# Optimization experiments

Hardware: AMD Instinct MI355X
Metric: run time of the kernel (lower is better)

Reference implementation:

```python
import jax, jax.numpy as jnp
import numpy as np
import math

H, D = 8, 16
O = H * D  # out_channels = 128
N_TYPES = 2
EDGE_META = [(0, 1), (1, 0)]  # (src_type, dst_type) per edge type: user->item, item->user

def _segment_softmax(alpha, dst, n):
    # PyG softmax over incoming edges grouped by destination node
    amax = jax.ops.segment_max(alpha, dst, num_segments=n)
    amax = jnp.where(jnp.isfinite(amax), amax, 0.0)
    ex = jnp.exp(alpha - amax[dst])
    den = jax.ops.segment_sum(ex, dst, num_segments=n)
    return ex / (den[dst] + 1e-16)

def setup_inputs():
    key = jax.random.key(0)
    ks = jax.random.split(key, 8)
    N, E, I = 50000, 500000, 128
    s = 1.0 / math.sqrt(I)
    sd = 1.0 / math.sqrt(D)
    return {
        "x": jax.random.normal(ks[0], (N_TYPES, N, I), jnp.float32),
        "k_w": jax.random.normal(ks[1], (N_TYPES, O, I), jnp.float32) * s,
        "k_b": jnp.zeros((N_TYPES, O), jnp.float32),
        "q_w": jax.random.normal(ks[2], (N_TYPES, O, I), jnp.float32) * s,
        "q_b": jnp.zeros((N_TYPES, O), jnp.float32),
        "v_w": jax.random.normal(ks[3], (N_TYPES, O, I), jnp.float32) * s,
        "v_b": jnp.zeros((N_TYPES, O), jnp.float32),
        "a_w": jax.random.normal(ks[4], (N_TYPES, O, O), jnp.float32) * s,
        "a_b": jnp.zeros((N_TYPES, O), jnp.float32),
        "skip": jnp.ones((N_TYPES,), jnp.float32),
        "a_rel": jax.random.normal(ks[5], (2, H, D, D), jnp.float32) * sd,
        "m_rel": jax.random.normal(ks[6], (2, H, D, D), jnp.float32) * sd,
        "p_rel": jnp.ones((2, H), jnp.float32),
        "ln_g": jnp.ones((O,), jnp.float32),
        "ln_b": jnp.zeros((O,), jnp.float32),
        "edge_index": jax.random.randint(ks[7], (2, 2, E), 0, N, jnp.int32),
    }

def reference(x, k_w, k_b, q_w, q_b, v_w, v_b, a_w, a_b, skip, a_rel, m_rel, p_rel, ln_g, ln_b, edge_index):
    N = x.shape[1]
    lin = lambda xi, w, b: xi @ w.T + b
    # per-node-type K/Q/V projections -> [T, N, H, D]
    k = jnp.stack([lin(x[t], k_w[t], k_b[t]) for t in range(N_TYPES)]).reshape(N_TYPES, N, H, D)
    q = jnp.stack([lin(x[t], q_w[t], q_b[t]) for t in range(N_TYPES)]).reshape(N_TYPES, N, H, D)
    v = jnp.stack([lin(x[t], v_w[t], v_b[t]) for t in range(N_TYPES)]).reshape(N_TYPES, N, H, D)
    agg = jnp.zeros((N_TYPES, N, O), x.dtype)
    for e, (st, dt) in enumerate(EDGE_META):
        src, dst = edge_index[e, 0], edge_index[e, 1]
        ke = jnp.einsum('nhd,hde->nhe', k[st], a_rel[e])  # relation-transformed keys
        ve = jnp.einsum('nhd,hde->nhe', v[st], m_rel[e])  # relation-transformed values
        alpha = jnp.einsum('ehd,ehd->eh', q[dt][dst], ke[src]) * p_rel[e] / math.sqrt(D)
        alpha = _segment_softmax(alpha, dst, N)  # [E, H]
        msg = (ve[src] * alpha[..., None]).reshape(-1, O)
        agg = agg.at[dt].add(jax.ops.segment_sum(msg, dst, num_segments=N))
    outs = []
    for t in range(N_TYPES):
        o = lin(jax.nn.gelu(agg[t], approximate=False), a_w[t], a_b[t])
        beta = jax.nn.sigmoid(skip[t])
        o = beta * o + (1.0 - beta) * x[t]  # HGT skip (out_channels == in_channels)
        o = jax.nn.relu(o)
        mu = jnp.mean(o, axis=-1, keepdims=True)
        var = jnp.mean((o - mu) ** 2, axis=-1, keepdims=True)
        o = (o - mu) / jnp.sqrt(var + 1e-5) * ln_g + ln_b  # LayerNorm; dropout = identity (eval)
        outs.append(o)
    return jnp.stack(outs)  # [2, N, 128]
```

## Files before the change

kernel.cpp:

```cpp
#include <hip/hip_runtime.h>
#include <math.h>


#define EB_STRIDE 40

typedef __attribute__((ext_vector_type(8))) short short8;
typedef __attribute__((ext_vector_type(4))) float floatx4;

__device__ __forceinline__ float bf2f(unsigned int bits16) {
  union { unsigned int i; float f; } u; u.i = bits16 << 16; return u.f;
}
__device__ __forceinline__ float bf2f_hi(unsigned int u) {
  union { unsigned int i; float f; } v; v.i = u & 0xffff0000u; return v.f;
}
__device__ __forceinline__ unsigned short f2bf(float f) {
  union { float ff; unsigned int i; } u; u.ff = f;
  unsigned int x = u.i;
  x += 0x7fffu + ((x >> 16) & 1u);
  return (unsigned short)(x >> 16);
}

__global__ void fuse_weights(
    const float* __restrict__ k_w, const float* __restrict__ k_b,
    const float* __restrict__ q_w, const float* __restrict__ q_b,
    const float* __restrict__ v_w, const float* __restrict__ v_b,
    const float* __restrict__ a_w, const float* __restrict__ a_b,
    const float* __restrict__ a_rel, const float* __restrict__ m_rel,
    const float* __restrict__ p_rel,
    unsigned short* __restrict__ Wfb, float* __restrict__ Bf)
{
  int tid = blockIdx.x * 256 + threadIdx.x;
  if (tid >= 2 * 4 * 128 * 128) return;
  int t   = tid >> 16;
  int rem = tid & 65535;
  int m   = rem >> 14;
  int o   = (rem >> 7) & 127;
  int i   = rem & 127;
  float w, bias;
  if (m == 0) {
    w    = q_w[t * 16384 + o * 128 + i];
    bias = q_b[t * 128 + o];
  } else if (m == 3) {
    w    = a_w[t * 16384 + o * 128 + i];
    bias = a_b[t * 128 + o];
  } else {
    const float* bw  = (m == 1) ? k_w : v_w;
    const float* bb  = (m == 1) ? k_b : v_b;
    const float* rel = (m == 1) ? a_rel : m_rel;
    int h = o >> 4, eo = o & 15;
    float s = 0.f, sb = 0.f;
    #pragma unroll
    for (int d = 0; d < 16; ++d) {
      float r = rel[t * 2048 + h * 256 + d * 16 + eo];
      s  += bw[t * 16384 + (h * 16 + d) * 128 + i] * r;
      sb += bb[t * 128 + h * 16 + d] * r;
    }
    if (m == 1) {
      float sc = p_rel[t * 8 + h] * 0.25f;
      s *= sc; sb *= sc;
    }
    w = s; bias = sb;
  }
  Wfb[tid] = f2bf(w);
  if (i == 0) Bf[t * 512 + m * 128 + o] = bias;
}

__global__ void init_cnt(int* __restrict__ cnt, int nC)
{
  int tid = blockIdx.x * 256 + threadIdx.x;
  if (tid < nC) cnt[tid] = 0;
}

__global__ void fill_edges(const int* __restrict__ ei, int* __restrict__ cnt,
                           int* __restrict__ ebuf, int N, int E)
{
  int e = blockIdx.y;
  int i = blockIdx.x * 256 + threadIdx.x;
  if (i >= E) return;
  int src = ei[(size_t)e * 2 * E + i];
  int dst = ei[(size_t)e * 2 * E + E + i];
  int b = (1 - e) * N + dst;
  int pos = atomicAdd(&cnt[b], 1);
  if (pos < EB_STRIDE) ebuf[(size_t)b * EB_STRIDE + pos] = src;
}

__global__ __launch_bounds__(256) void gemm_qkv(
    const float* __restrict__ x, const unsigned short* __restrict__ Wfb,
    const float* __restrict__ Bf, unsigned short* __restrict__ qbuf,
    unsigned short* __restrict__ kvbuf, int Nn)
{
  __shared__ alignas(16) unsigned short Als[128][136];
  __shared__ alignas(16) unsigned short Bls[128][136];
  const int tid = threadIdx.x;
  const int t = blockIdx.y;
  const int m0 = blockIdx.x * 128;
  const int lane = tid & 63, w = tid >> 6;
  const int col = lane & 15, quad = lane >> 4;
  const int morder[3] = {1, 2, 0};

  {
    int r = tid & 127, h = tid >> 7;
    int gn = m0 + r;
    if (gn < Nn) {
      const float* ap = x + (size_t)t * Nn * 128 + (size_t)gn * 128 + h * 64;
      #pragma unroll
      for (int j = 0; j < 16; ++j) {
        float4 f = ((const float4*)ap)[j];
        ushort4 s;
        s.x = f2bf(f.x); s.y = f2bf(f.y); s.z = f2bf(f.z); s.w = f2bf(f.w);
        *(ushort4*)&Als[r][h * 64 + j * 4] = s;
      }
    } else {
      ushort4 z = make_ushort4(0, 0, 0, 0);
      #pragma unroll
      for (int j = 0; j < 16; ++j) *(ushort4*)&Als[r][h * 64 + j * 4] = z;
    }
  }

  float acc_k[2][8][4];
  float bias_n[8];

  for (int mi_ = 0; mi_ < 3; ++mi_) {
    int m = morder[mi_];
    __syncthreads();
    {
      int r = tid & 127, h = tid >> 7;
      const unsigned short* wp = Wfb + (((size_t)(t * 4 + m)) << 14) + r * 128 + h * 64;
      #pragma unroll
      for (int j = 0; j < 8; ++j)
        *(uint4*)&Bls[r][h * 64 + j * 8] = ((const uint4*)wp)[j];
    }
    __syncthreads();

    floatx4 acc[2][8];
    #pragma unroll
    for (int mi = 0; mi < 2; ++mi)
      #pragma unroll
      for (int ni = 0; ni < 8; ++ni) acc[mi][ni] = (floatx4)(0.f);

    #pragma unroll
    for (int k0 = 0; k0 < 128; k0 += 32) {
      int kk = k0 + quad * 8;
      short8 a0 = *(const short8*)&Als[w * 32 + col][kk];
      short8 a1 = *(const short8*)&Als[w * 32 + 16 + col][kk];
      #pragma unroll
      for (int ni = 0; ni < 8; ++ni) {
        short8 b = *(const short8*)&Bls[ni * 16 + col][kk];
        acc[0][ni] = __builtin_amdgcn_mfma_f32_16x16x32_bf16(a0, b, acc[0][ni], 0, 0, 0);
        acc[1][ni] = __builtin_amdgcn_mfma_f32_16x16x32_bf16(a1, b, acc[1][ni], 0, 0, 0);
      }
    }

    const float* Bv = Bf + t * 512 + m * 128;
    #pragma unroll
    for (int ni = 0; ni < 8; ++ni) bias_n[ni] = Bv[ni * 16 + col];

    if (m == 1) {
      #pragma unroll
      for (int mi = 0; mi < 2; ++mi)
        #pragma unroll
        for (int ni = 0; ni < 8; ++ni)
          #pragma unroll
          for (int reg = 0; reg < 4; ++reg)
            acc_k[mi][ni][reg] = acc[mi][ni][reg] + bias_n[ni];
    } else if (m == 2) {
      unsigned int* kvp = (unsigned int*)kvbuf + ((size_t)t * Nn) * 128;
      #pragma unroll
      for (int mi = 0; mi < 2; ++mi)
        #pragma unroll
        for (int reg = 0; reg < 4; ++reg) {
          int row = m0 + w * 32 + mi * 16 + quad * 4 + reg;
          if (row >= Nn) continue;
          unsigned int* cp = kvp + (size_t)row * 128 + col;
          #pragma unroll
          for (int ni = 0; ni < 8; ++ni) {
            unsigned int kbits = f2bf(acc_k[mi][ni][reg]);
            unsigned int vbits = f2bf(acc[mi][ni][reg] + bias_n[ni]);
            cp[ni * 16] = (vbits << 16) | kbits;
          }
        }
    } else {
      #pragma unroll
      for (int mi = 0; mi < 2; ++mi)
        #pragma unroll
        for (int reg = 0; reg < 4; ++reg) {
          int row = m0 + w * 32 + mi * 16 + quad * 4 + reg;
          if (row >= Nn) continue;
          unsigned short* cp = qbuf + ((size_t)t * Nn + row) * 128 + col;
          #pragma unroll
          for (int ni = 0; ni < 8; ++ni)
            cp[ni * 16] = f2bf(acc[mi][ni][reg] + bias_n[ni]);
        }
    }
  }
}

__global__ __launch_bounds__(256) void gather_fused(
    const unsigned short* __restrict__ qbuf, const unsigned short* __restrict__ kvbuf,
    const int* __restrict__ cnt, const int* __restrict__ ebuf,
    unsigned short* __restrict__ gbuf, int N)
{
  int wid = (blockIdx.x * 256 + threadIdx.x) >> 6;
  int l = threadIdx.x & 63;
  if (wid >= 2 * N) return;
  int dt = (wid >= N) ? 1 : 0;
  int e  = 1 - dt;
  int deg = cnt[wid]; if (deg > EB_STRIDE) deg = EB_STRIDE;
  int g = l >> 4, gl = l & 15;

  uint4 qr = *(const uint4*)(qbuf + (size_t)wid * 128 + 8 * gl);
  float qv[8];
  qv[0] = bf2f(qr.x & 0xffffu); qv[1] = bf2f(qr.x >> 16);
  qv[2] = bf2f(qr.y & 0xffffu); qv[3] = bf2f(qr.y >> 16);
  qv[4] = bf2f(qr.z & 0xffffu); qv[5] = bf2f(qr.z >> 16);
  qv[6] = bf2f(qr.w & 0xffffu); qv[7] = bf2f(qr.w >> 16);

  const unsigned short* kvbase = kvbuf + ((size_t)e * N) * 256;
  const int* eb = ebuf + (size_t)wid * EB_STRIDE;
  int mysrc = (l < deg) ? eb[l] : 0;

  float acc[8];
  #pragma unroll
  for (int c = 0; c < 8; ++c) acc[c] = 0.f;
  float den = 0.f;

  for (int j0 = 0; j0 < deg; j0 += 4) {
    int j = j0 + g;
    bool valid = j < deg;
    int src = __shfl(mysrc, valid ? j : 0, 64);
    const unsigned short* kv = kvbase + (size_t)src * 256 + 16 * gl;
    uint4 a = *(const uint4*)kv;
    uint4 b = *(const uint4*)(kv + 8);
    float p;
    p = qv[0] * bf2f(a.x & 0xffffu);
    p = fmaf(qv[1], bf2f(a.y & 0xffffu), p);
    p = fmaf(qv[2], bf2f(a.z & 0xffffu), p);
    p = fmaf(qv[3], bf2f(a.w & 0xffffu), p);
    p = fmaf(qv[4], bf2f(b.x & 0xffffu), p);
    p = fmaf(qv[5], bf2f(b.y & 0xffffu), p);
    p = fmaf(qv[6], bf2f(b.z & 0xffffu), p);
    p = fmaf(qv[7], bf2f(b.w & 0xffffu), p);
    float pt = p + __shfl_xor(p, 1, 64);
    float ex = valid ? __expf(pt) : 0.f;
    den += ex;
    acc[0] = fmaf(ex, bf2f_hi(a.x), acc[0]);
    acc[1] = fmaf(ex, bf2f_hi(a.y), acc[1]);
    acc[2] = fmaf(ex, bf2f_hi(a.z), acc[2]);
    acc[3] = fmaf(ex, bf2f_hi(a.w), acc[3]);
    acc[4] = fmaf(ex, bf2f_hi(b.x), acc[4]);
    acc[5] = fmaf(ex, bf2f_hi(b.y), acc[5]);
    acc[6] = fmaf(ex, bf2f_hi(b.z), acc[6]);
    acc[7] = fmaf(ex, bf2f_hi(b.w), acc[7]);
  }

  #pragma unroll
  for (int off = 16; off < 64; off <<= 1) {
    #pragma unroll
    for (int c = 0; c < 8; ++c) acc[c] += __shfl_xor(acc[c], off, 64);
    den += __shfl_xor(den, off, 64);
  }

  if (g == 0) {
    float rden = 1.f / (den + 1e-16f);
    unsigned short r[8];
    #pragma unroll
    for (int c = 0; c < 8; ++c) {
      float gg = acc[c] * rden;
      r[c] = f2bf(0.5f * gg * (1.f + erff(gg * 0.70710678118654752f)));
    }
    unsigned short* op = gbuf + (size_t)wid * 128 + 8 * gl;
    *(ushort4*)op       = make_ushort4(r[0], r[1], r[2], r[3]);
    *(ushort4*)(op + 4) = make_ushort4(r[4], r[5], r[6], r[7]);
  }
}

__global__ __launch_bounds__(256) void gemm_ln(
    const unsigned short* __restrict__ gbuf, const unsigned short* __restrict__ Wfb,
    const float* __restrict__ Bf, const float* __restrict__ x,
    const float* __restrict__ skip, const float* __restrict__ ln_g,
    const float* __restrict__ ln_b, float* __restrict__ outp, int Nn)
{
  __shared__ alignas(16) unsigned short Als[128][136];
  __shared__ alignas(16) unsigned short Bls[128][136];
  const int tid = threadIdx.x;
  const int t = blockIdx.y;
  const int m0 = blockIdx.x * 128;
  const int lane = tid & 63, w = tid >> 6;
  const int col = lane & 15, quad = lane >> 4;

  {
    int r = tid & 127, h = tid >> 7;
    int gn = m0 + r;
    if (gn < Nn) {
      const unsigned short* ap = gbuf + (size_t)t * Nn * 128 + (size_t)gn * 128 + h * 64;
      #pragma unroll
      for (int j = 0; j < 8; ++j)
        *(uint4*)&Als[r][h * 64 + j * 8] = ((const uint4*)ap)[j];
    } else {
      uint4 z = make_uint4(0, 0, 0, 0);
      #pragma unroll
      for (int j = 0; j < 8; ++j) *(uint4*)&Als[r][h * 64 + j * 8] = z;
    }
  }
  {
    int r = tid & 127, h = tid >> 7;
    const unsigned short* wp = Wfb + (((size_t)(t * 4 + 3)) << 14) + r * 128 + h * 64;
    #pragma unroll
    for (int j = 0; j < 8; ++j)
      *(uint4*)&Bls[r][h * 64 + j * 8] = ((const uint4*)wp)[j];
  }
  __syncthreads();

  floatx4 acc[2][8];
  #pragma unroll
  for (int mi = 0; mi < 2; ++mi)
    #pragma unroll
    for (int ni = 0; ni < 8; ++ni) acc[mi][ni] = (floatx4)(0.f);

  #pragma unroll
  for (int k0 = 0; k0 < 128; k0 += 32) {
    int kk = k0 + quad * 8;
    short8 a0 = *(const short8*)&Als[w * 32 + col][kk];
    short8 a1 = *(const short8*)&Als[w * 32 + 16 + col][kk];
    #pragma unroll
    for (int ni = 0; ni < 8; ++ni) {
      short8 b = *(const short8*)&Bls[ni * 16 + col][kk];
      acc[0][ni] = __builtin_amdgcn_mfma_f32_16x16x32_bf16(a0, b, acc[0][ni], 0, 0, 0);
      acc[1][ni] = __builtin_amdgcn_mfma_f32_16x16x32_bf16(a1, b, acc[1][ni], 0, 0, 0);
    }
  }

  const float* Bv = Bf + t * 512 + 3 * 128;
  float bias_n[8], g_n[8], b_n[8];
  #pragma unroll
  for (int ni = 0; ni < 8; ++ni) {
    bias_n[ni] = Bv[ni * 16 + col];
    g_n[ni]    = ln_g[ni * 16 + col];
    b_n[ni]    = ln_b[ni * 16 + col];
  }
  float sv = skip[t];
  float beta = 1.f / (1.f + __expf(-sv));
  const float* xt = x + (size_t)t * Nn * 128;
  float* op = outp + (size_t)t * Nn * 128;

  #pragma unroll
  for (int mi = 0; mi < 2; ++mi)
    #pragma unroll
    for (int reg = 0; reg < 4; ++reg) {
      int row = m0 + w * 32 + mi * 16 + quad * 4 + reg;
      if (row >= Nn) continue;
      const float* xr = xt + (size_t)row * 128;
      float vals[8], s = 0.f;
      #pragma unroll
      for (int ni = 0; ni < 8; ++ni) {
        float o = acc[mi][ni][reg] + bias_n[ni];
        float v = fmaxf(beta * o + (1.f - beta) * xr[ni * 16 + col], 0.f);
        vals[ni] = v; s += v;
      }
      #pragma unroll
      for (int off = 1; off < 16; off <<= 1) s += __shfl_xor(s, off, 64);
      float mu = s * 0.0078125f;
      float sq = 0.f;
      #pragma unroll
      for (int ni = 0; ni < 8; ++ni) { float d = vals[ni] - mu; sq += d * d; }
      #pragma unroll
      for (int off = 1; off < 16; off <<= 1) sq += __shfl_xor(sq, off, 64);
      float rstd = rsqrtf(sq * 0.0078125f + 1e-5f);
      float* orow = op + (size_t)row * 128 + col;
      #pragma unroll
      for (int ni = 0; ni < 8; ++ni)
        orow[ni * 16] = (vals[ni] - mu) * rstd * g_n[ni] + b_n[ni];
    }
}

extern "C" void kernel_launch(void* const* d_in, const int* in_sizes, int n_in,
                              void* d_out, int out_size, void* d_ws, size_t ws_size,
                              hipStream_t stream) {
  const float* x     = (const float*)d_in[0];
  const float* k_w   = (const float*)d_in[1];
  const float* k_b   = (const float*)d_in[2];
  const float* q_w   = (const float*)d_in[3];
  const float* q_b   = (const float*)d_in[4];
  const float* v_w   = (const float*)d_in[5];
  const float* v_b   = (const float*)d_in[6];
  const float* a_w   = (const float*)d_in[7];
  const float* a_b   = (const float*)d_in[8];
  const float* skip  = (const float*)d_in[9];
  const float* a_rel = (const float*)d_in[10];
  const float* m_rel = (const float*)d_in[11];
  const float* p_rel = (const float*)d_in[12];
  const float* ln_g  = (const float*)d_in[13];
  const float* ln_b  = (const float*)d_in[14];
  const int* ei      = (const int*)d_in[15];
  float* out         = (float*)d_out;

  const int N = in_sizes[0] / 256;
  const int E = in_sizes[15] / 4;

  unsigned short* Wfb = (unsigned short*)d_ws;
  float* Bf = (float*)(Wfb + 2 * 4 * 128 * 128);
  unsigned short* qbuf = (unsigned short*)(Bf + 2 * 4 * 128);
  unsigned short* kvbuf = qbuf + (size_t)2 * N * 128;
  int* cnt  = (int*)(kvbuf + (size_t)2 * N * 256);
  int* ebuf = cnt + (size_t)2 * N;
  unsigned short* gbuf = (unsigned short*)(ebuf + (size_t)2 * N * EB_STRIDE);

  fuse_weights<<<(2 * 4 * 128 * 128 + 255) / 256, 256, 0, stream>>>(
      k_w, k_b, q_w, q_b, v_w, v_b, a_w, a_b, a_rel, m_rel, p_rel, Wfb, Bf);

  init_cnt<<<(2 * N + 255) / 256, 256, 0, stream>>>(cnt, 2 * N);

  fill_edges<<<dim3((E + 255) / 256, 2), 256, 0, stream>>>(ei, cnt, ebuf, N, E);

  int Mb = (N + 127) / 128;
  gemm_qkv<<<dim3(Mb, 2), 256, 0, stream>>>(x, Wfb, Bf, qbuf, kvbuf, N);

  gather_fused<<<(2 * N * 64 + 255) / 256, 256, 0, stream>>>(
      qbuf, kvbuf, cnt, ebuf, gbuf, N);

  gemm_ln<<<dim3(Mb, 2), 256, 0, stream>>>(
      gbuf, Wfb, Bf, x, skip, ln_g, ln_b, out, N);
}
```

Measured before the change: 324.9 us.

## Fuse edge bucketing into QKV GEMM launch and halve GEMM row tiles

Folds the counter zeroing into fuse_weights and runs edge bucketing as extra blocks of the QKV GEMM kernel, which cuts two launches and lets the atomic-heavy fill overlap the GEMM. Both GEMM kernels shrink their M tile from 128 to 64 rows and use a 1D grid, giving more blocks and less LDS per block for better occupancy. The trade-off is that each 128x128 weight tile is reloaded per 64-row block, and fill blocks now compete with GEMM blocks for compute units.

```diff
diff --git a/kernel.cpp b/kernel.cpp
--- a/kernel.cpp
+++ b/kernel.cpp
@@ -27,9 +27,11 @@
     const float* __restrict__ a_w, const float* __restrict__ a_b,
     const float* __restrict__ a_rel, const float* __restrict__ m_rel,
     const float* __restrict__ p_rel,
-    unsigned short* __restrict__ Wfb, float* __restrict__ Bf)
+    unsigned short* __restrict__ Wfb, float* __restrict__ Bf,
+    int* __restrict__ cnt, int nC)
 {
   int tid = blockIdx.x * 256 + threadIdx.x;
+  if (tid < nC) cnt[tid] = 0;
   if (tid >= 2 * 4 * 128 * 128) return;
   int t   = tid >> 16;
   int rem = tid & 65535;
@@ -65,59 +67,58 @@
   if (i == 0) Bf[t * 512 + m * 128 + o] = bias;
 }
 
-__global__ void init_cnt(int* __restrict__ cnt, int nC)
-{
-  int tid = blockIdx.x * 256 + threadIdx.x;
-  if (tid < nC) cnt[tid] = 0;
-}
-
-__global__ void fill_edges(const int* __restrict__ ei, int* __restrict__ cnt,
-                           int* __restrict__ ebuf, int N, int E)
-{
-  int e = blockIdx.y;
-  int i = blockIdx.x * 256 + threadIdx.x;
-  if (i >= E) return;
-  int src = ei[(size_t)e * 2 * E + i];
-  int dst = ei[(size_t)e * 2 * E + E + i];
-  int b = (1 - e) * N + dst;
-  int pos = atomicAdd(&cnt[b], 1);
-  if (pos < EB_STRIDE) ebuf[(size_t)b * EB_STRIDE + pos] = src;
-}
-
-__global__ __launch_bounds__(256) void gemm_qkv(
+__global__ __launch_bounds__(256) void qkv_fill(
     const float* __restrict__ x, const unsigned short* __restrict__ Wfb,
     const float* __restrict__ Bf, unsigned short* __restrict__ qbuf,
-    unsigned short* __restrict__ kvbuf, int Nn)
+    unsigned short* __restrict__ kvbuf,
+    const int* __restrict__ ei, int* __restrict__ cnt, int* __restrict__ ebuf,
+    int Nn, int E, int Gg)
 {
-  __shared__ alignas(16) unsigned short Als[128][136];
+  __shared__ alignas(16) unsigned short Als[64][136];
   __shared__ alignas(16) unsigned short Bls[128][136];
+  const int b = blockIdx.x;
   const int tid = threadIdx.x;
-  const int t = blockIdx.y;
-  const int m0 = blockIdx.x * 128;
+
+  if (b >= Gg) {
+    int f = b - Gg;
+    int e = f & 1;
+    int i = (f >> 1) * 256 + tid;
+    if (i < E) {
+      int src = ei[(size_t)e * 2 * E + i];
+      int dst = ei[(size_t)e * 2 * E + E + i];
+      int bk = (1 - e) * Nn + dst;
+      int pos = atomicAdd(&cnt[bk], 1);
+      if (pos < EB_STRIDE) ebuf[(size_t)bk * EB_STRIDE + pos] = src;
+    }
+    return;
+  }
+
+  const int t = b & 1;
+  const int m0 = (b >> 1) * 64;
   const int lane = tid & 63, w = tid >> 6;
   const int col = lane & 15, quad = lane >> 4;
   const int morder[3] = {1, 2, 0};
 
   {
-    int r = tid & 127, h = tid >> 7;
+    int r = tid & 63, h = tid >> 6;
     int gn = m0 + r;
     if (gn < Nn) {
-      const float* ap = x + (size_t)t * Nn * 128 + (size_t)gn * 128 + h * 64;
-      #pragma unroll
-      for (int j = 0; j < 16; ++j) {
+      const float* ap = x + (size_t)t * Nn * 128 + (size_t)gn * 128 + h * 32;
+      #pragma unroll
+      for (int j = 0; j < 8; ++j) {
         float4 f = ((const float4*)ap)[j];
         ushort4 s;
         s.x = f2bf(f.x); s.y = f2bf(f.y); s.z = f2bf(f.z); s.w = f2bf(f.w);
-        *(ushort4*)&Als[r][h * 64 + j * 4] = s;
+        *(ushort4*)&Als[r][h * 32 + j * 4] = s;
       }
     } else {
       ushort4 z = make_ushort4(0, 0, 0, 0);
       #pragma unroll
-      for (int j = 0; j < 16; ++j) *(ushort4*)&Als[r][h * 64 + j * 4] = z;
-    }
-  }
-
-  float acc_k[2][8][4];
+      for (int j = 0; j < 8; ++j) *(ushort4*)&Als[r][h * 32 + j * 4] = z;
+    }
+  }
+
+  float acc_k[8][4];
   float bias_n[8];
 
   for (int mi_ = 0; mi_ < 3; ++mi_) {
@@ -132,22 +133,18 @@
     }
     __syncthreads();
 
-    floatx4 acc[2][8];
-    #pragma unroll
-    for (int mi = 0; mi < 2; ++mi)
-      #pragma unroll
-      for (int ni = 0; ni < 8; ++ni) acc[mi][ni] = (floatx4)(0.f);
+    floatx4 acc[8];
+    #pragma unroll
+    for (int ni = 0; ni < 8; ++ni) acc[ni] = (floatx4)(0.f);
 
     #pragma unroll
     for (int k0 = 0; k0 < 128; k0 += 32) {
       int kk = k0 + quad * 8;
-      short8 a0 = *(const short8*)&Als[w * 32 + col][kk];
-      short8 a1 = *(const short8*)&Als[w * 32 + 16 + col][kk];
+      short8 a0 = *(const short8*)&Als[w * 16 + col][kk];
       #pragma unroll
       for (int ni = 0; ni < 8; ++ni) {
-        short8 b = *(const short8*)&Bls[ni * 16 + col][kk];
-        acc[0][ni] = __builtin_amdgcn_mfma_f32_16x16x32_bf16(a0, b, acc[0][ni], 0, 0, 0);
-        acc[1][ni] = __builtin_amdgcn_mfma_f32_16x16x32_bf16(a1, b, acc[1][ni], 0, 0, 0);
+        short8 bb = *(const short8*)&Bls[ni * 16 + col][kk];
+        acc[ni] = __builtin_amdgcn_mfma_f32_16x16x32_bf16(a0, bb, acc[ni], 0, 0, 0);
       }
     }
 
@@ -157,40 +154,34 @@
 
     if (m == 1) {
       #pragma unroll
-      for (int mi = 0; mi < 2; ++mi)
+      for (int ni = 0; ni < 8; ++ni)
+        #pragma unroll
+        for (int reg = 0; reg < 4; ++reg)
+          acc_k[ni][reg] = acc[ni][reg] + bias_n[ni];
+    } else if (m == 2) {
+      unsigned int* kvp = (unsigned int*)kvbuf + ((size_t)t * Nn) * 128;
+      #pragma unroll
+      for (int reg = 0; reg < 4; ++reg) {
+        int row = m0 + w * 16 + quad * 4 + reg;
+        if (row >= Nn) continue;
+        unsigned int* cp = kvp + (size_t)row * 128 + col;
+        #pragma unroll
+        for (int ni = 0; ni < 8; ++ni) {
+          unsigned int kbits = f2bf(acc_k[ni][reg]);
+          unsigned int vbits = f2bf(acc[ni][reg] + bias_n[ni]);
+          cp[ni * 16] = (vbits << 16) | kbits;
+        }
+      }
+    } else {
+      #pragma unroll
+      for (int reg = 0; reg < 4; ++reg) {
+        int row = m0 + w * 16 + quad * 4 + reg;
+        if (row >= Nn) continue;
+        unsigned short* cp = qbuf + ((size_t)t * Nn + row) * 128 + col;
         #pragma unroll
         for (int ni = 0; ni < 8; ++ni)
-          #pragma unroll
-          for (int reg = 0; reg < 4; ++reg)
-            acc_k[mi][ni][reg] = acc[mi][ni][reg] + bias_n[ni];
-    } else if (m == 2) {
-      unsigned int* kvp = (unsigned int*)kvbuf + ((size_t)t * Nn) * 128;
-      #pragma unroll
-      for (int mi = 0; mi < 2; ++mi)
-        #pragma unroll
-        for (int reg = 0; reg < 4; ++reg) {
-          int row = m0 + w * 32 + mi * 16 + quad * 4 + reg;
-          if (row >= Nn) continue;
-          unsigned int* cp = kvp + (size_t)row * 128 + col;
-          #pragma unroll
-          for (int ni = 0; ni < 8; ++ni) {
-            unsigned int kbits = f2bf(acc_k[mi][ni][reg]);
-            unsigned int vbits = f2bf(acc[mi][ni][reg] + bias_n[ni]);
-            cp[ni * 16] = (vbits << 16) | kbits;
-          }
-        }
-    } else {
-      #pragma unroll
-      for (int mi = 0; mi < 2; ++mi)
-        #pragma unroll
-        for (int reg = 0; reg < 4; ++reg) {
-          int row = m0 + w * 32 + mi * 16 + quad * 4 + reg;
-          if (row >= Nn) continue;
-          unsigned short* cp = qbuf + ((size_t)t * Nn + row) * 128 + col;
-          #pragma unroll
-          for (int ni = 0; ni < 8; ++ni)
-            cp[ni * 16] = f2bf(acc[mi][ni][reg] + bias_n[ni]);
-        }
+          cp[ni * 16] = f2bf(acc[ni][reg] + bias_n[ni]);
+      }
     }
   }
 }
@@ -280,26 +271,26 @@
     const float* __restrict__ skip, const float* __restrict__ ln_g,
     const float* __restrict__ ln_b, float* __restrict__ outp, int Nn)
 {
-  __shared__ alignas(16) unsigned short Als[128][136];
+  __shared__ alignas(16) unsigned short Als[64][136];
   __shared__ alignas(16) unsigned short Bls[128][136];
   const int tid = threadIdx.x;
-  const int t = blockIdx.y;
-  const int m0 = blockIdx.x * 128;
+  const int t = blockIdx.x & 1;
+  const int m0 = (blockIdx.x >> 1) * 64;
   const int lane = tid & 63, w = tid >> 6;
   const int col = lane & 15, quad = lane >> 4;
 
   {
-    int r = tid & 127, h = tid >> 7;
+    int r = tid & 63, h = tid >> 6;
     int gn = m0 + r;
     if (gn < Nn) {
-      const unsigned short* ap = gbuf + (size_t)t * Nn * 128 + (size_t)gn * 128 + h * 64;
-      #pragma unroll
-      for (int j = 0; j < 8; ++j)
-        *(uint4*)&Als[r][h * 64 + j * 8] = ((const uint4*)ap)[j];
+      const unsigned short* ap = gbuf + (size_t)t * Nn * 128 + (size_t)gn * 128 + h * 32;
+      #pragma unroll
+      for (int j = 0; j < 4; ++j)
+        *(uint4*)&Als[r][h * 32 + j * 8] = ((const uint4*)ap)[j];
     } else {
       uint4 z = make_uint4(0, 0, 0, 0);
       #pragma unroll
-      for (int j = 0; j < 8; ++j) *(uint4*)&Als[r][h * 64 + j * 8] = z;
+      for (int j = 0; j < 4; ++j) *(uint4*)&Als[r][h * 32 + j * 8] = z;
     }
   }
   {
@@ -311,22 +302,18 @@
   }
   __syncthreads();
 
-  floatx4 acc[2][8];
-  #pragma unroll
-  for (int mi = 0; mi < 2; ++mi)
-    #pragma unroll
-    for (int ni = 0; ni < 8; ++ni) acc[mi][ni] = (floatx4)(0.f);
+  floatx4 acc[8];
+  #pragma unroll
+  for (int ni = 0; ni < 8; ++ni) acc[ni] = (floatx4)(0.f);
 
   #pragma unroll
   for (int k0 = 0; k0 < 128; k0 += 32) {
     int kk = k0 + quad * 8;
-    short8 a0 = *(const short8*)&Als[w * 32 + col][kk];
-    short8 a1 = *(const short8*)&Als[w * 32 + 16 + col][kk];
+    short8 a0 = *(const short8*)&Als[w * 16 + col][kk];
     #pragma unroll
     for (int ni = 0; ni < 8; ++ni) {
-      short8 b = *(const short8*)&Bls[ni * 16 + col][kk];
-      acc[0][ni] = __builtin_amdgcn_mfma_f32_16x16x32_bf16(a0, b, acc[0][ni], 0, 0, 0);
-      acc[1][ni] = __builtin_amdgcn_mfma_f32_16x16x32_bf16(a1, b, acc[1][ni], 0, 0, 0);
+      short8 bb = *(const short8*)&Bls[ni * 16 + col][kk];
+      acc[ni] = __builtin_amdgcn_mfma_f32_16x16x32_bf16(a0, bb, acc[ni], 0, 0, 0);
     }
   }
 
@@ -344,33 +331,31 @@
   float* op = outp + (size_t)t * Nn * 128;
 
   #pragma unroll
-  for (int mi = 0; mi < 2; ++mi)
-    #pragma unroll
-    for (int reg = 0; reg < 4; ++reg) {
-      int row = m0 + w * 32 + mi * 16 + quad * 4 + reg;
-      if (row >= Nn) continue;
-      const float* xr = xt + (size_t)row * 128;
-      float vals[8], s = 0.f;
-      #pragma unroll
-      for (int ni = 0; ni < 8; ++ni) {
-        float o = acc[mi][ni][reg] + bias_n[ni];
-        float v = fmaxf(beta * o + (1.f - beta) * xr[ni * 16 + col], 0.f);
-        vals[ni] = v; s += v;
-      }
-      #pragma unroll
-      for (int off = 1; off < 16; off <<= 1) s += __shfl_xor(s, off, 64);
-      float mu = s * 0.0078125f;
-      float sq = 0.f;
-      #pragma unroll
-      for (int ni = 0; ni < 8; ++ni) { float d = vals[ni] - mu; sq += d * d; }
-      #pragma unroll
-      for (int off = 1; off < 16; off <<= 1) sq += __shfl_xor(sq, off, 64);
-      float rstd = rsqrtf(sq * 0.0078125f + 1e-5f);
-      float* orow = op + (size_t)row * 128 + col;
-      #pragma unroll
-      for (int ni = 0; ni < 8; ++ni)
-        orow[ni * 16] = (vals[ni] - mu) * rstd * g_n[ni] + b_n[ni];
-    }
+  for (int reg = 0; reg < 4; ++reg) {
+    int row = m0 + w * 16 + quad * 4 + reg;
+    if (row >= Nn) continue;
+    const float* xr = xt + (size_t)row * 128;
+    float vals[8], s = 0.f;
+    #pragma unroll
+    for (int ni = 0; ni < 8; ++ni) {
+      float o = acc[ni][reg] + bias_n[ni];
+      float v = fmaxf(beta * o + (1.f - beta) * xr[ni * 16 + col], 0.f);
+      vals[ni] = v; s += v;
+    }
+    #pragma unroll
+    for (int off = 1; off < 16; off <<= 1) s += __shfl_xor(s, off, 64);
+    float mu = s * 0.0078125f;
+    float sq = 0.f;
+    #pragma unroll
+    for (int ni = 0; ni < 8; ++ni) { float d = vals[ni] - mu; sq += d * d; }
+    #pragma unroll
+    for (int off = 1; off < 16; off <<= 1) sq += __shfl_xor(sq, off, 64);
+    float rstd = rsqrtf(sq * 0.0078125f + 1e-5f);
+    float* orow = op + (size_t)row * 128 + col;
+    #pragma unroll
+    for (int ni = 0; ni < 8; ++ni)
+      orow[ni * 16] = (vals[ni] - mu) * rstd * g_n[ni] + b_n[ni];
+  }
 }
 
 extern "C" void kernel_launch(void* const* d_in, const int* in_sizes, int n_in,
@@ -406,18 +391,18 @@
   unsigned short* gbuf = (unsigned short*)(ebuf + (size_t)2 * N * EB_STRIDE);
 
   fuse_weights<<<(2 * 4 * 128 * 128 + 255) / 256, 256, 0, stream>>>(
-      k_w, k_b, q_w, q_b, v_w, v_b, a_w, a_b, a_rel, m_rel, p_rel, Wfb, Bf);
-
-  init_cnt<<<(2 * N + 255) / 256, 256, 0, stream>>>(cnt, 2 * N);
-
-  fill_edges<<<dim3((E + 255) / 256, 2), 256, 0, stream>>>(ei, cnt, ebuf, N, E);
-
-  int Mb = (N + 127) / 128;
-  gemm_qkv<<<dim3(Mb, 2), 256, 0, stream>>>(x, Wfb, Bf, qbuf, kvbuf, N);
+      k_w, k_b, q_w, q_b, v_w, v_b, a_w, a_b, a_rel, m_rel, p_rel, Wfb, Bf,
+      cnt, 2 * N);
+
+  int Mb64 = (N + 63) / 64;
+  int Gg = Mb64 * 2;
+  int Fb = 2 * ((E + 255) / 256);
+  qkv_fill<<<Gg + Fb, 256, 0, stream>>>(
+      x, Wfb, Bf, qbuf, kvbuf, ei, cnt, ebuf, N, E, Gg);
 
   gather_fused<<<(2 * N * 64 + 255) / 256, 256, 0, stream>>>(
       qbuf, kvbuf, cnt, ebuf, gbuf, N);
 
-  gemm_ln<<<dim3(Mb, 2), 256, 0, stream>>>(
+  gemm_ln<<<Gg, 256, 0, stream>>>(
       gbuf, Wfb, Bf, x, skip, ln_g, ln_b, out, N);
 }
```

After: 301.8 us. 1.08x faster.

## Merge count init into weight fusion and run edge bucketing alongside QKV GEMM

Applied to the files above, without the earlier changes.

The kernel that zeroes the per-node edge counters is folded into fuse_weights, which has enough threads to cover 2N counters (131072 threads vs 100000). The edge bucketing pass is merged into the QKV GEMM launch: extra blocks beyond the GEMM grid perform the atomic bucket fill, so memory-bound atomics can overlap with the MFMA GEMM blocks. Grids are flattened to 1D with interleaved node types. This removes two launches and their serialization, but the fill blocks share the launch with LDS-heavy GEMM blocks and compete with them for resources.

```diff
diff --git a/kernel.cpp b/kernel.cpp
--- a/kernel.cpp
+++ b/kernel.cpp
@@ -27,9 +27,11 @@
     const float* __restrict__ a_w, const float* __restrict__ a_b,
     const float* __restrict__ a_rel, const float* __restrict__ m_rel,
     const float* __restrict__ p_rel,
-    unsigned short* __restrict__ Wfb, float* __restrict__ Bf)
+    unsigned short* __restrict__ Wfb, float* __restrict__ Bf,
+    int* __restrict__ cnt, int nC)
 {
   int tid = blockIdx.x * 256 + threadIdx.x;
+  if (tid < nC) cnt[tid] = 0;
   if (tid >= 2 * 4 * 128 * 128) return;
   int t   = tid >> 16;
   int rem = tid & 65535;
@@ -65,35 +67,34 @@
   if (i == 0) Bf[t * 512 + m * 128 + o] = bias;
 }
 
-__global__ void init_cnt(int* __restrict__ cnt, int nC)
-{
-  int tid = blockIdx.x * 256 + threadIdx.x;
-  if (tid < nC) cnt[tid] = 0;
-}
-
-__global__ void fill_edges(const int* __restrict__ ei, int* __restrict__ cnt,
-                           int* __restrict__ ebuf, int N, int E)
-{
-  int e = blockIdx.y;
-  int i = blockIdx.x * 256 + threadIdx.x;
-  if (i >= E) return;
-  int src = ei[(size_t)e * 2 * E + i];
-  int dst = ei[(size_t)e * 2 * E + E + i];
-  int b = (1 - e) * N + dst;
-  int pos = atomicAdd(&cnt[b], 1);
-  if (pos < EB_STRIDE) ebuf[(size_t)b * EB_STRIDE + pos] = src;
-}
-
-__global__ __launch_bounds__(256) void gemm_qkv(
+__global__ __launch_bounds__(256) void qkv_fill(
     const float* __restrict__ x, const unsigned short* __restrict__ Wfb,
     const float* __restrict__ Bf, unsigned short* __restrict__ qbuf,
-    unsigned short* __restrict__ kvbuf, int Nn)
+    unsigned short* __restrict__ kvbuf,
+    const int* __restrict__ ei, int* __restrict__ cnt, int* __restrict__ ebuf,
+    int Nn, int E, int Gg)
 {
   __shared__ alignas(16) unsigned short Als[128][136];
   __shared__ alignas(16) unsigned short Bls[128][136];
+  const int b = blockIdx.x;
   const int tid = threadIdx.x;
-  const int t = blockIdx.y;
-  const int m0 = blockIdx.x * 128;
+
+  if (b >= Gg) {
+    int f = b - Gg;
+    int e = f & 1;
+    int i = (f >> 1) * 256 + tid;
+    if (i < E) {
+      int src = ei[(size_t)e * 2 * E + i];
+      int dst = ei[(size_t)e * 2 * E + E + i];
+      int bk = (1 - e) * Nn + dst;
+      int pos = atomicAdd(&cnt[bk], 1);
+      if (pos < EB_STRIDE) ebuf[(size_t)bk * EB_STRIDE + pos] = src;
+    }
+    return;
+  }
+
+  const int t = b & 1;
+  const int m0 = (b >> 1) * 128;
   const int lane = tid & 63, w = tid >> 6;
   const int col = lane & 15, quad = lane >> 4;
   const int morder[3] = {1, 2, 0};
@@ -145,9 +146,9 @@
       short8 a1 = *(const short8*)&Als[w * 32 + 16 + col][kk];
       #pragma unroll
       for (int ni = 0; ni < 8; ++ni) {
-        short8 b = *(const short8*)&Bls[ni * 16 + col][kk];
-        acc[0][ni] = __builtin_amdgcn_mfma_f32_16x16x32_bf16(a0, b, acc[0][ni], 0, 0, 0);
-        acc[1][ni] = __builtin_amdgcn_mfma_f32_16x16x32_bf16(a1, b, acc[1][ni], 0, 0, 0);
+        short8 bb = *(const short8*)&Bls[ni * 16 + col][kk];
+        acc[0][ni] = __builtin_amdgcn_mfma_f32_16x16x32_bf16(a0, bb, acc[0][ni], 0, 0, 0);
+        acc[1][ni] = __builtin_amdgcn_mfma_f32_16x16x32_bf16(a1, bb, acc[1][ni], 0, 0, 0);
       }
     }
 
@@ -283,8 +284,8 @@
   __shared__ alignas(16) unsigned short Als[128][136];
   __shared__ alignas(16) unsigned short Bls[128][136];
   const int tid = threadIdx.x;
-  const int t = blockIdx.y;
-  const int m0 = blockIdx.x * 128;
+  const int t = blockIdx.x & 1;
+  const int m0 = (blockIdx.x >> 1) * 128;
   const int lane = tid & 63, w = tid >> 6;
   const int col = lane & 15, quad = lane >> 4;
 
@@ -324,9 +325,9 @@
     short8 a1 = *(const short8*)&Als[w * 32 + 16 + col][kk];
     #pragma unroll
     for (int ni = 0; ni < 8; ++ni) {
-      short8 b = *(const short8*)&Bls[ni * 16 + col][kk];
-      acc[0][ni] = __builtin_amdgcn_mfma_f32_16x16x32_bf16(a0, b, acc[0][ni], 0, 0, 0);
-      acc[1][ni] = __builtin_amdgcn_mfma_f32_16x16x32_bf16(a1, b, acc[1][ni], 0, 0, 0);
+      short8 bb = *(const short8*)&Bls[ni * 16 + col][kk];
+      acc[0][ni] = __builtin_amdgcn_mfma_f32_16x16x32_bf16(a0, bb, acc[0][ni], 0, 0, 0);
+      acc[1][ni] = __builtin_amdgcn_mfma_f32_16x16x32_bf16(a1, bb, acc[1][ni], 0, 0, 0);
     }
   }
 
@@ -406,18 +407,18 @@
   unsigned short* gbuf = (unsigned short*)(ebuf + (size_t)2 * N * EB_STRIDE);
 
   fuse_weights<<<(2 * 4 * 128 * 128 + 255) / 256, 256, 0, stream>>>(
-      k_w, k_b, q_w, q_b, v_w, v_b, a_w, a_b, a_rel, m_rel, p_rel, Wfb, Bf);
-
-  init_cnt<<<(2 * N + 255) / 256, 256, 0, stream>>>(cnt, 2 * N);
-
-  fill_edges<<<dim3((E + 255) / 256, 2), 256, 0, stream>>>(ei, cnt, ebuf, N, E);
+      k_w, k_b, q_w, q_b, v_w, v_b, a_w, a_b, a_rel, m_rel, p_rel, Wfb, Bf,
+      cnt, 2 * N);
 
   int Mb = (N + 127) / 128;
-  gemm_qkv<<<dim3(Mb, 2), 256, 0, stream>>>(x, Wfb, Bf, qbuf, kvbuf, N);
+  int Gg = Mb * 2;
+  int Fb = 2 * ((E + 255) / 256);
+  qkv_fill<<<Gg + Fb, 256, 0, stream>>>(
+      x, Wfb, Bf, qbuf, kvbuf, ei, cnt, ebuf, N, E, Gg);
 
   gather_fused<<<(2 * N * 64 + 255) / 256, 256, 0, stream>>>(
       qbuf, kvbuf, cnt, ebuf, gbuf, N);
 
-  gemm_ln<<<dim3(Mb, 2), 256, 0, stream>>>(
+  gemm_ln<<<Gg, 256, 0, stream>>>(
       gbuf, Wfb, Bf, x, skip, ln_g, ln_b, out, N);
 }
```

Measured after the change: 297.7 us. -8.4%, faster.
